# Kernel optimization log

Hardware: AMD Instinct MI355X
Metric: run time of the kernel (lower is better)

Reference implementation:

```python
import jax, jax.numpy as jnp
import numpy as np

DT = 0.001
BATCH, INPUT_SIZE, HIDDEN_SIZE, T = 32, 16384, 1024, 10


def setup_inputs() -> dict:
    key = jax.random.key(0)
    k1, k2, k3 = jax.random.split(key, 3)
    input_spikes = (jax.random.uniform(k1, (BATCH, INPUT_SIZE, T)) < 0.1).astype(jnp.float32)
    weight = jax.random.normal(k2, (INPUT_SIZE, HIDDEN_SIZE), dtype=jnp.float32) * 0.1
    synaptic_strength = jnp.ones((INPUT_SIZE, HIDDEN_SIZE), jnp.float32)
    threshold = jnp.ones((HIDDEN_SIZE,), jnp.float32)  # threshold_init = 1.0
    firing_rate_estimate = jnp.zeros((HIDDEN_SIZE,), jnp.float32)
    return {
        "input_spikes": input_spikes,
        "weight": weight,
        "synaptic_strength": synaptic_strength,
        "threshold": threshold,
        "firing_rate_estimate": firing_rate_estimate,
        "tau_mem": jnp.float32(0.02),
        "tau_syn": jnp.float32(0.005),
        "target_rate": jnp.float32(0.1),
        "homeostatic_lr": jnp.float32(0.001),
        "time_steps": T,
    }


def reference(input_spikes, weight, synaptic_strength, threshold,
              firing_rate_estimate, tau_mem, tau_syn, target_rate,
              homeostatic_lr, time_steps):
    # input_spikes: [B, I, T]; eval mode (no stochastic STDP branch)
    B = input_spikes.shape[0]
    H = threshold.shape[0]
    alpha_mem = jnp.exp(-DT / tau_mem)
    alpha_syn = jnp.exp(-DT / tau_syn)
    # precompute the per-step weighted input once: [T, B, H]
    w_eff = weight * synaptic_strength
    weighted = jnp.einsum('bit,ih->tbh', input_spikes[..., :time_steps], w_eff)

    def step(carry, w_in):
        v, i, fre, thr = carry
        i = alpha_syn * i + w_in
        v = alpha_mem * v + i
        spikes = (v >= thr[None, :]).astype(v.dtype)
        v = v - spikes * thr[None, :]  # reset_mode='subtract'
        spike_rate = spikes.mean(axis=0)
        fre = 0.99 * fre + 0.01 * spike_rate
        thr = thr + homeostatic_lr * (fre - target_rate)  # homeostatic adaptation
        diag = (v.mean(), spike_rate.mean(), thr.mean())
        return (v, i, fre, thr), (spikes, diag)

    init = (jnp.zeros((B, H), input_spikes.dtype),
            jnp.zeros((B, H), input_spikes.dtype),
            firing_rate_estimate, threshold)
    _, (spikes_tbh, (mem_means, rate_means, thr_means)) = jax.lax.scan(step, init, weighted)
    output_spikes = jnp.transpose(spikes_tbh, (1, 2, 0))  # [B, H, T]
    return output_spikes, mem_means, rate_means, thr_means
```

## Files before the change

### kernel.cpp

```cpp
#include <hip/hip_runtime.h>
#include <stdint.h>

#define B_ 32
#define I_ 16384
#define H_ 1024
#define T_ 10
#define M_ 320
#define NW 32

typedef __attribute__((ext_vector_type(8))) short short8;
typedef __attribute__((ext_vector_type(4))) float f32x4;
typedef __attribute__((ext_vector_type(4))) unsigned int u32x4;

__global__ __launch_bounds__(256) void pack_s(const float* __restrict__ spikes,
                                              uint16_t* __restrict__ Sbf) {
  __shared__ __align__(16) uint16_t tile[M_ * 40];
  const int i0 = blockIdx.x * 32;
#pragma unroll
  for (int p = 0; p < 10; p++) {
    int e = p * 256 + threadIdx.x;
    int b = e / 80;
    int r = e - b * 80;
    f32x4 val = *(const f32x4*)&spikes[(size_t)b * (I_ * T_) + (size_t)i0 * T_ + r * 4];
#pragma unroll
    for (int j = 0; j < 4; j++) {
      int pos = r * 4 + j;
      int il = pos / 10;
      int t = pos - il * 10;
      float f = (j == 0) ? val.x : (j == 1) ? val.y : (j == 2) ? val.z : val.w;
      union { float f; unsigned int u; } cv; cv.f = f;
      tile[(t * 32 + b) * 40 + il] = (uint16_t)(cv.u >> 16);
    }
  }
  __syncthreads();
#pragma unroll
  for (int p = 0; p < 5; p++) {
    int e = p * 256 + threadIdx.x;
    int m = e >> 2, il8 = e & 3;
    u32x4 w = *(const u32x4*)&tile[m * 40 + il8 * 8];
    *(u32x4*)&Sbf[(size_t)m * I_ + i0 + il8 * 8] = w;
  }
}

__global__ __launch_bounds__(640, 5) void gemm(const uint16_t* __restrict__ Sbf,
                                               const float* __restrict__ Wg,
                                               const float* __restrict__ Sg,
                                               float* __restrict__ partial,
                                               int kchunk) {
  __shared__ __align__(16) uint16_t WhiL[2][4 * NW * 40];
  __shared__ __align__(16) uint16_t WloL[2][4 * NW * 40];

  const int nt = blockIdx.x & 31;
  const int ks = blockIdx.x >> 5;
  const int nbase = nt * NW;
  const int tid = threadIdx.x;
  const int lane = tid & 63, wid = tid >> 6;
  const int quad = lane >> 4, l15 = lane & 15;

  const int stages = kchunk >> 7;
  const int kofs = ks * kchunk;

  const uint16_t* aptr0 = Sbf + (size_t)(wid * 32 + l15) * I_ + quad * 8;
  const uint16_t* aptr1 = aptr0 + (size_t)16 * I_;

  const int wn = tid & 31;
  const int wko = (tid >> 5) & 15;

  f32x4 acc[2][2];
#pragma unroll
  for (int a = 0; a < 2; a++)
#pragma unroll
    for (int b = 0; b < 2; b++) acc[a][b] = f32x4{0.f, 0.f, 0.f, 0.f};

  u32x4 afC[2], afN[2];
  float wpre[8], spre[8];

#define BAR()                                                               \
  do {                                                                      \
    asm volatile("s_waitcnt lgkmcnt(0)" ::: "memory");                      \
    __builtin_amdgcn_s_barrier();                                           \
    __builtin_amdgcn_sched_barrier(0);                                      \
  } while (0)

#define PACK_W(pn)                                                          \
  if (tid < 512) {                                                          \
    unsigned int hw[4], lw[4];                                              \
    _Pragma("unroll")                                                       \
    for (int j2 = 0; j2 < 4; j2++) {                                        \
      unsigned int hh[2], ll[2];                                            \
      _Pragma("unroll")                                                     \
      for (int e = 0; e < 2; e++) {                                         \
        float p = wpre[j2 * 2 + e] * spre[j2 * 2 + e];                      \
        union { float f; unsigned int u; } cv; cv.f = p;                    \
        unsigned int hb = (cv.u + 0x7FFFu + ((cv.u >> 16) & 1u)) >> 16;     \
        union { unsigned int u; float f; } hv; hv.u = hb << 16;             \
        float lo = p - hv.f;                                                \
        union { float f; unsigned int u; } cl; cl.f = lo;                   \
        unsigned int lb = (cl.u + 0x7FFFu + ((cl.u >> 16) & 1u)) >> 16;     \
        hh[e] = hb; ll[e] = lb;                                             \
      }                                                                     \
      hw[j2] = hh[0] | (hh[1] << 16);                                       \
      lw[j2] = ll[0] | (ll[1] << 16);                                       \
    }                                                                       \
    int wofs = (wko >> 2) * (NW * 40) + wn * 40 + (wko & 3) * 8;            \
    *(u32x4*)&WhiL[pn][wofs] = u32x4{hw[0], hw[1], hw[2], hw[3]};           \
    *(u32x4*)&WloL[pn][wofs] = u32x4{lw[0], lw[1], lw[2], lw[3]};           \
  }

#define LOAD_W(kb)                                                          \
  if (tid < 512) {                                                          \
    _Pragma("unroll")                                                       \
    for (int j = 0; j < 8; j++) {                                           \
      size_t g = (size_t)((kb) + wko * 8 + j) * H_ + nbase + wn;            \
      wpre[j] = Wg[g]; spre[j] = Sg[g];                                     \
    }                                                                       \
  }

  afC[0] = *(const u32x4*)(aptr0 + kofs);
  afC[1] = *(const u32x4*)(aptr1 + kofs);
  LOAD_W(kofs);
  PACK_W(0);
  if (stages > 1) LOAD_W(kofs + (1 << 7));
  BAR();

  const int lastA = stages * 4 - 1;
  for (int s = 0; s < stages; ++s) {
    const int pc = s & 1;
#pragma unroll
    for (int ku = 0; ku < 4; ++ku) {
      int nidx = s * 4 + ku + 1;
      if (nidx > lastA) nidx = lastA;
      const int nkb = kofs + nidx * 32;
      afN[0] = *(const u32x4*)(aptr0 + nkb);
      afN[1] = *(const u32x4*)(aptr1 + nkb);
      short8 a0 = __builtin_bit_cast(short8, afC[0]);
      short8 a1 = __builtin_bit_cast(short8, afC[1]);
#pragma unroll
      for (int tn = 0; tn < 2; ++tn) {
        int n = tn * 16 + l15;
        short8 bhi = *(const short8*)&WhiL[pc][ku * (NW * 40) + n * 40 + quad * 8];
        short8 blo = *(const short8*)&WloL[pc][ku * (NW * 40) + n * 40 + quad * 8];
        acc[0][tn] = __builtin_amdgcn_mfma_f32_16x16x32_bf16(a0, bhi, acc[0][tn], 0, 0, 0);
        acc[0][tn] = __builtin_amdgcn_mfma_f32_16x16x32_bf16(a0, blo, acc[0][tn], 0, 0, 0);
        acc[1][tn] = __builtin_amdgcn_mfma_f32_16x16x32_bf16(a1, bhi, acc[1][tn], 0, 0, 0);
        acc[1][tn] = __builtin_amdgcn_mfma_f32_16x16x32_bf16(a1, blo, acc[1][tn], 0, 0, 0);
      }
      afC[0] = afN[0]; afC[1] = afN[1];
    }
    if (s + 1 < stages) {
      PACK_W(pc ^ 1);
      if (s + 2 < stages) LOAD_W(kofs + ((s + 2) << 7));
      BAR();
    }
  }

#pragma unroll
  for (int tm = 0; tm < 2; tm++)
#pragma unroll
    for (int tn = 0; tn < 2; tn++) {
      int mrow = wid * 32 + tm * 16 + quad * 4;
      int ncol = nbase + tn * 16 + l15;
      float* dst = partial + ((size_t)ks * M_ + mrow) * H_ + ncol;
      dst[0 * H_] = acc[tm][tn].x;
      dst[1 * H_] = acc[tm][tn].y;
      dst[2 * H_] = acc[tm][tn].z;
      dst[3 * H_] = acc[tm][tn].w;
    }
#undef PACK_W
#undef LOAD_W
#undef BAR
}

__global__ __launch_bounds__(256) void reduce_w(const float* __restrict__ partial,
                                                float* __restrict__ weighted,
                                                float* __restrict__ out, int KS) {
  if (blockIdx.x == 0 && threadIdx.x < 30) out[327680 + threadIdx.x] = 0.f;
  int j = (blockIdx.x * 256 + threadIdx.x) * 4;
  f32x4 s = f32x4{0.f, 0.f, 0.f, 0.f};
  for (int k = 0; k < KS; k++) {
    f32x4 p = *(const f32x4*)&partial[(size_t)k * (M_ * H_) + j];
    s += p;
  }
  *(f32x4*)&weighted[j] = s;
}

__global__ __launch_bounds__(64) void scan(const float* __restrict__ weighted,
                                           const float* __restrict__ threshold,
                                           const float* __restrict__ fre0,
                                           const float* __restrict__ p_tau_mem,
                                           const float* __restrict__ p_tau_syn,
                                           const float* __restrict__ p_target,
                                           const float* __restrict__ p_lr,
                                           float* __restrict__ out) {
  const int lane = threadIdx.x;
  const int hl = lane & 15, bg = lane >> 4;
  const int h = blockIdx.x * 16 + hl;
  const float alpha_mem = expf(-0.001f / p_tau_mem[0]);
  const float alpha_syn = expf(-0.001f / p_tau_syn[0]);
  const float target = p_target[0], lr = p_lr[0];
  float v[8], isyn[8];
#pragma unroll
  for (int j = 0; j < 8; j++) { v[j] = 0.f; isyn[j] = 0.f; }
  float fre = fre0[h];
  float thr = threshold[h];
  for (int t = 0; t < T_; t++) {
    float rsum = 0.f, vsum = 0.f;
#pragma unroll
    for (int j = 0; j < 8; j++) {
      int b = bg * 8 + j;
      float w_in = weighted[(size_t)(t * 32 + b) * H_ + h];
      isyn[j] = alpha_syn * isyn[j] + w_in;
      v[j] = alpha_mem * v[j] + isyn[j];
      float spike = (v[j] >= thr) ? 1.f : 0.f;
      v[j] -= spike * thr;
      out[(size_t)b * (H_ * T_) + (size_t)h * T_ + t] = spike;
      rsum += spike;
      vsum += v[j];
    }
    float r = rsum;
    r += __shfl_xor(r, 16);
    r += __shfl_xor(r, 32);
    float rate = r * (1.f / 32.f);
    fre = 0.99f * fre + 0.01f * rate;
    thr = thr + lr * (fre - target);
    float vv = vsum, rr = rate, tt = thr;
#pragma unroll
    for (int off = 32; off >= 1; off >>= 1) {
      vv += __shfl_xor(vv, off);
      rr += __shfl_xor(rr, off);
      tt += __shfl_xor(tt, off);
    }
    if (lane == 0) {
      atomicAdd(&out[327680 + t], vv * (1.f / 32768.f));
      atomicAdd(&out[327690 + t], rr * (1.f / 4096.f));
      atomicAdd(&out[327700 + t], tt * (1.f / 4096.f));
    }
  }
}

extern "C" void kernel_launch(void* const* d_in, const int* in_sizes, int n_in,
                              void* d_out, int out_size, void* d_ws, size_t ws_size,
                              hipStream_t stream) {
  const float* spikes    = (const float*)d_in[0];
  const float* weight    = (const float*)d_in[1];
  const float* strength  = (const float*)d_in[2];
  const float* threshold = (const float*)d_in[3];
  const float* fre0      = (const float*)d_in[4];
  const float* tau_mem   = (const float*)d_in[5];
  const float* tau_syn   = (const float*)d_in[6];
  const float* target    = (const float*)d_in[7];
  const float* lr        = (const float*)d_in[8];
  float* out = (float*)d_out;

  const size_t sbf_bytes = (size_t)M_ * I_ * 2;
  const size_t slice     = (size_t)M_ * H_ * 4;
  int KS = 16;
  while (KS > 1 && sbf_bytes + (size_t)(KS + 1) * slice > ws_size) KS >>= 1;

  uint16_t* Sbf   = (uint16_t*)d_ws;
  float* partial  = (float*)((char*)d_ws + sbf_bytes);
  float* weighted = (float*)((char*)d_ws + sbf_bytes + (size_t)KS * slice);

  pack_s<<<I_ / 32, 256, 0, stream>>>(spikes, Sbf);
  gemm<<<32 * KS, 640, 0, stream>>>(Sbf, weight, strength, partial, I_ / KS);
  reduce_w<<<(M_ * H_) / 1024, 256, 0, stream>>>(partial, weighted, out, KS);
  scan<<<H_ / 16, 64, 0, stream>>>(weighted, threshold, fre0, tau_mem, tau_syn,
                                   target, lr, out);
}
```

Before: 243.5 us.

## Widen GEMM N-tile to 128, shrink K-stage, double split-K, spread scan

The GEMM block now covers 128 hidden columns with a 32-wide K stage instead of 32 columns with a 128-wide K stage. Each A fragment loaded from global memory therefore feeds 8 N-subtiles instead of 2, which cuts redundant reads of the packed spike matrix. Split-K goes from 16 to 32, and the block index now puts ks in the low bits, so blocks sharing a K range run next to each other. The scan kernel uses 4 hidden units per block instead of 16 to spread the sequential recurrence over more blocks. The costs are more accumulator registers (launch-bounds occupancy drops from 5 to 3), a barrier every 32 K, a larger partial-sum buffer for the reduce kernel, and more atomics in the scan.

```diff
diff --git a/kernel.cpp b/kernel.cpp
--- a/kernel.cpp
+++ b/kernel.cpp
@@ -6,7 +6,8 @@
 #define H_ 1024
 #define T_ 10
 #define M_ 320
-#define NW 32
+#define NW 128
+#define BK 32
 
 typedef __attribute__((ext_vector_type(8))) short short8;
 typedef __attribute__((ext_vector_type(4))) float f32x4;
@@ -42,37 +43,37 @@
   }
 }
 
-__global__ __launch_bounds__(640, 5) void gemm(const uint16_t* __restrict__ Sbf,
+__global__ __launch_bounds__(640, 3) void gemm(const uint16_t* __restrict__ Sbf,
                                                const float* __restrict__ Wg,
                                                const float* __restrict__ Sg,
                                                float* __restrict__ partial,
-                                               int kchunk) {
-  __shared__ __align__(16) uint16_t WhiL[2][4 * NW * 40];
-  __shared__ __align__(16) uint16_t WloL[2][4 * NW * 40];
-
-  const int nt = blockIdx.x & 31;
-  const int ks = blockIdx.x >> 5;
+                                               int kchunk, int KS) {
+  __shared__ __align__(16) uint16_t WhiL[2][NW * 40];
+  __shared__ __align__(16) uint16_t WloL[2][NW * 40];
+
+  const int ks = blockIdx.x % KS;
+  const int nt = blockIdx.x / KS;
   const int nbase = nt * NW;
   const int tid = threadIdx.x;
   const int lane = tid & 63, wid = tid >> 6;
   const int quad = lane >> 4, l15 = lane & 15;
 
-  const int stages = kchunk >> 7;
+  const int stages = kchunk >> 5;
   const int kofs = ks * kchunk;
 
   const uint16_t* aptr0 = Sbf + (size_t)(wid * 32 + l15) * I_ + quad * 8;
   const uint16_t* aptr1 = aptr0 + (size_t)16 * I_;
 
-  const int wn = tid & 31;
-  const int wko = (tid >> 5) & 15;
-
-  f32x4 acc[2][2];
+  const int wn = tid & 127;
+  const int wko = (tid >> 7) & 3;
+
+  f32x4 acc[2][8];
 #pragma unroll
   for (int a = 0; a < 2; a++)
 #pragma unroll
-    for (int b = 0; b < 2; b++) acc[a][b] = f32x4{0.f, 0.f, 0.f, 0.f};
-
-  u32x4 afC[2], afN[2];
+    for (int b = 0; b < 8; b++) acc[a][b] = f32x4{0.f, 0.f, 0.f, 0.f};
+
+  u32x4 af[2];
   float wpre[8], spre[8];
 
 #define BAR()                                                               \
@@ -102,7 +103,7 @@
       hw[j2] = hh[0] | (hh[1] << 16);                                       \
       lw[j2] = ll[0] | (ll[1] << 16);                                       \
     }                                                                       \
-    int wofs = (wko >> 2) * (NW * 40) + wn * 40 + (wko & 3) * 8;            \
+    int wofs = wn * 40 + wko * 8;                                           \
     *(u32x4*)&WhiL[pn][wofs] = u32x4{hw[0], hw[1], hw[2], hw[3]};           \
     *(u32x4*)&WloL[pn][wofs] = u32x4{lw[0], lw[1], lw[2], lw[3]};           \
   }
@@ -116,40 +117,40 @@
     }                                                                       \
   }
 
-  afC[0] = *(const u32x4*)(aptr0 + kofs);
-  afC[1] = *(const u32x4*)(aptr1 + kofs);
+#define ISSUE_A(kb)                                                         \
+  {                                                                         \
+    af[0] = *(const u32x4*)(aptr0 + (kb));                                  \
+    af[1] = *(const u32x4*)(aptr1 + (kb));                                  \
+  }
+
+#define COMPUTE(pc)                                                         \
+  {                                                                         \
+    short8 a0 = __builtin_bit_cast(short8, af[0]);                          \
+    short8 a1 = __builtin_bit_cast(short8, af[1]);                          \
+    _Pragma("unroll")                                                       \
+    for (int tn = 0; tn < 8; ++tn) {                                        \
+      int n = tn * 16 + l15;                                                \
+      short8 bhi = *(const short8*)&WhiL[pc][n * 40 + quad * 8];            \
+      short8 blo = *(const short8*)&WloL[pc][n * 40 + quad * 8];            \
+      acc[0][tn] = __builtin_amdgcn_mfma_f32_16x16x32_bf16(a0, bhi, acc[0][tn], 0, 0, 0); \
+      acc[0][tn] = __builtin_amdgcn_mfma_f32_16x16x32_bf16(a0, blo, acc[0][tn], 0, 0, 0); \
+      acc[1][tn] = __builtin_amdgcn_mfma_f32_16x16x32_bf16(a1, bhi, acc[1][tn], 0, 0, 0); \
+      acc[1][tn] = __builtin_amdgcn_mfma_f32_16x16x32_bf16(a1, blo, acc[1][tn], 0, 0, 0); \
+    }                                                                       \
+  }
+
   LOAD_W(kofs);
+  ISSUE_A(kofs);
   PACK_W(0);
-  if (stages > 1) LOAD_W(kofs + (1 << 7));
+  if (stages > 1) LOAD_W(kofs + BK);
   BAR();
 
-  const int lastA = stages * 4 - 1;
   for (int s = 0; s < stages; ++s) {
-    const int pc = s & 1;
-#pragma unroll
-    for (int ku = 0; ku < 4; ++ku) {
-      int nidx = s * 4 + ku + 1;
-      if (nidx > lastA) nidx = lastA;
-      const int nkb = kofs + nidx * 32;
-      afN[0] = *(const u32x4*)(aptr0 + nkb);
-      afN[1] = *(const u32x4*)(aptr1 + nkb);
-      short8 a0 = __builtin_bit_cast(short8, afC[0]);
-      short8 a1 = __builtin_bit_cast(short8, afC[1]);
-#pragma unroll
-      for (int tn = 0; tn < 2; ++tn) {
-        int n = tn * 16 + l15;
-        short8 bhi = *(const short8*)&WhiL[pc][ku * (NW * 40) + n * 40 + quad * 8];
-        short8 blo = *(const short8*)&WloL[pc][ku * (NW * 40) + n * 40 + quad * 8];
-        acc[0][tn] = __builtin_amdgcn_mfma_f32_16x16x32_bf16(a0, bhi, acc[0][tn], 0, 0, 0);
-        acc[0][tn] = __builtin_amdgcn_mfma_f32_16x16x32_bf16(a0, blo, acc[0][tn], 0, 0, 0);
-        acc[1][tn] = __builtin_amdgcn_mfma_f32_16x16x32_bf16(a1, bhi, acc[1][tn], 0, 0, 0);
-        acc[1][tn] = __builtin_amdgcn_mfma_f32_16x16x32_bf16(a1, blo, acc[1][tn], 0, 0, 0);
-      }
-      afC[0] = afN[0]; afC[1] = afN[1];
-    }
+    COMPUTE(s & 1);
     if (s + 1 < stages) {
-      PACK_W(pc ^ 1);
-      if (s + 2 < stages) LOAD_W(kofs + ((s + 2) << 7));
+      ISSUE_A(kofs + (s + 1) * BK);
+      PACK_W((s + 1) & 1);
+      if (s + 2 < stages) LOAD_W(kofs + (s + 2) * BK);
       BAR();
     }
   }
@@ -157,7 +158,7 @@
 #pragma unroll
   for (int tm = 0; tm < 2; tm++)
 #pragma unroll
-    for (int tn = 0; tn < 2; tn++) {
+    for (int tn = 0; tn < 8; tn++) {
       int mrow = wid * 32 + tm * 16 + quad * 4;
       int ncol = nbase + tn * 16 + l15;
       float* dst = partial + ((size_t)ks * M_ + mrow) * H_ + ncol;
@@ -168,6 +169,8 @@
     }
 #undef PACK_W
 #undef LOAD_W
+#undef ISSUE_A
+#undef COMPUTE
 #undef BAR
 }
 
@@ -193,21 +196,21 @@
                                            const float* __restrict__ p_lr,
                                            float* __restrict__ out) {
   const int lane = threadIdx.x;
-  const int hl = lane & 15, bg = lane >> 4;
-  const int h = blockIdx.x * 16 + hl;
+  const int hl = lane & 3, bg = lane >> 2;
+  const int h = blockIdx.x * 4 + hl;
   const float alpha_mem = expf(-0.001f / p_tau_mem[0]);
   const float alpha_syn = expf(-0.001f / p_tau_syn[0]);
   const float target = p_target[0], lr = p_lr[0];
-  float v[8], isyn[8];
-#pragma unroll
-  for (int j = 0; j < 8; j++) { v[j] = 0.f; isyn[j] = 0.f; }
+  float v[2], isyn[2];
+#pragma unroll
+  for (int j = 0; j < 2; j++) { v[j] = 0.f; isyn[j] = 0.f; }
   float fre = fre0[h];
   float thr = threshold[h];
   for (int t = 0; t < T_; t++) {
     float rsum = 0.f, vsum = 0.f;
 #pragma unroll
-    for (int j = 0; j < 8; j++) {
-      int b = bg * 8 + j;
+    for (int j = 0; j < 2; j++) {
+      int b = bg * 2 + j;
       float w_in = weighted[(size_t)(t * 32 + b) * H_ + h];
       isyn[j] = alpha_syn * isyn[j] + w_in;
       v[j] = alpha_mem * v[j] + isyn[j];
@@ -218,6 +221,8 @@
       vsum += v[j];
     }
     float r = rsum;
+    r += __shfl_xor(r, 4);
+    r += __shfl_xor(r, 8);
     r += __shfl_xor(r, 16);
     r += __shfl_xor(r, 32);
     float rate = r * (1.f / 32.f);
@@ -232,8 +237,8 @@
     }
     if (lane == 0) {
       atomicAdd(&out[327680 + t], vv * (1.f / 32768.f));
-      atomicAdd(&out[327690 + t], rr * (1.f / 4096.f));
-      atomicAdd(&out[327700 + t], tt * (1.f / 4096.f));
+      atomicAdd(&out[327690 + t], rr * (1.f / 16384.f));
+      atomicAdd(&out[327700 + t], tt * (1.f / 16384.f));
     }
   }
 }
@@ -254,7 +259,7 @@
 
   const size_t sbf_bytes = (size_t)M_ * I_ * 2;
   const size_t slice     = (size_t)M_ * H_ * 4;
-  int KS = 16;
+  int KS = 32;
   while (KS > 1 && sbf_bytes + (size_t)(KS + 1) * slice > ws_size) KS >>= 1;
 
   uint16_t* Sbf   = (uint16_t*)d_ws;
@@ -262,8 +267,9 @@
   float* weighted = (float*)((char*)d_ws + sbf_bytes + (size_t)KS * slice);
 
   pack_s<<<I_ / 32, 256, 0, stream>>>(spikes, Sbf);
-  gemm<<<32 * KS, 640, 0, stream>>>(Sbf, weight, strength, partial, I_ / KS);
+  gemm<<<(H_ / NW) * KS, 640, 0, stream>>>(Sbf, weight, strength, partial,
+                                           I_ / KS, KS);
   reduce_w<<<(M_ * H_) / 1024, 256, 0, stream>>>(partial, weighted, out, KS);
-  scan<<<H_ / 16, 64, 0, stream>>>(weighted, threshold, fre0, tau_mem, tau_syn,
-                                   target, lr, out);
-}
+  scan<<<H_ / 4, 64, 0, stream>>>(weighted, threshold, fre0, tau_mem, tau_syn,
+                                  target, lr, out);
+}
```

After: 258.7 us. 6.2% more time.
